# Optimization experiments

Measured on AMD Instinct MI355X. Metric: run time of the kernel, lower is better.

## Reference

```python
import jax, jax.numpy as jnp
import numpy as np

D_MODEL = 1024
NUM_HEADS = 16
OUT_SHAPE = (64,)            # ControlGate `shape`; d_head = prod(OUT_SHAPE)
BANK_SIZE = 16
TOP_K = 2
BATCH, SEQ = 8, 4096
D_OUT = NUM_HEADS * int(np.prod(OUT_SHAPE))  # 1024


def setup_inputs() -> dict:
    key = jax.random.key(0)
    k1, k2, k3, k4 = jax.random.split(key, 4)
    tensor = jax.random.normal(k1, (BATCH, SEQ, D_MODEL), dtype=jnp.float32)
    sel_idx = jax.random.randint(k2, (BATCH, TOP_K), 0, BANK_SIZE)
    sel_probs = jax.random.uniform(k3, (BATCH, TOP_K), dtype=jnp.float32)
    sel_probs = sel_probs / jnp.sum(sel_probs, axis=-1, keepdims=True)
    W = jax.random.normal(k4, (BANK_SIZE, D_MODEL, D_OUT), dtype=jnp.float32) * 0.02
    b = jnp.zeros((BANK_SIZE, D_OUT), dtype=jnp.float32)
    return {"tensor": tensor, "sel_idx": sel_idx, "sel_probs": sel_probs, "W": W, "b": b}


def reference(tensor, sel_idx, sel_probs, W, b):
    # --- VirtualMakeHeads: bank-selected (virtual) linear projection ---
    # Superimpose the selected weight banks per batch element.
    W_sel = W[sel_idx]                    # (B, K, d_model, d_out)  irregular gather
    b_sel = b[sel_idx]                    # (B, K, d_out)
    W_eff = jnp.einsum('bk,bkio->bio', sel_probs, W_sel)   # (B, d_model, d_out)
    b_eff = jnp.einsum('bk,bko->bo', sel_probs, b_sel)     # (B, d_out)
    logits = jnp.einsum('bsi,bio->bso', tensor, W_eff) + b_eff[:, None, :]
    # reshape to heads: (B, S, num_heads, d_head)
    logits = logits.reshape(*logits.shape[:-1], NUM_HEADS, -1)
    # --- ControlGate: unflatten last dim into OUT_SHAPE ---
    logits = logits.reshape(*logits.shape[:-1], *OUT_SHAPE)
    # DropoutLogits with p=0.0 (eval) is identity.
    # activation == 'sigmoid'
    return jax.nn.sigmoid(logits)
```

## Files before the change

kernel.cpp:

```cpp
#include <hip/hip_runtime.h>
#include <hip/hip_bf16.h>

#define B_  8
#define S_  4096
#define DM  1024
#define DO  1024

typedef __attribute__((ext_vector_type(4))) float f32x4;
typedef __attribute__((ext_vector_type(8))) short bf16x8;

__device__ inline unsigned int pkbf(float a, float b) {
    __hip_bfloat162 h = __float22bfloat162_rn(float2{a, b});
    union { __hip_bfloat162 h2; unsigned int u; } cv;
    cv.h2 = h;
    return cv.u;
}


__global__ __launch_bounds__(256) void prep_xpack(
    const float* __restrict__ X, unsigned short* __restrict__ xpack)
{
    const int kt = blockIdx.x, bm = blockIdx.y, b = blockIdx.z;
    const int r = threadIdx.x;
    const float* src = X + ((size_t)(b * S_ + bm * 256 + r)) * DM + kt * 64;
    char* dst = (char*)xpack + ((size_t)((b * 16 + bm) * 16 + kt)) * 32768 + r * 128;
    const int rx = r & 7;
    #pragma unroll
    for (int g = 0; g < 8; ++g) {
        float4 a = *reinterpret_cast<const float4*>(src + g * 8);
        float4 c = *reinterpret_cast<const float4*>(src + g * 8 + 4);
        uint4 u;
        u.x = pkbf(a.x, a.y); u.y = pkbf(a.z, a.w);
        u.z = pkbf(c.x, c.y); u.w = pkbf(c.z, c.w);
        *reinterpret_cast<uint4*>(dst + ((g ^ rx) << 4)) = u;
    }
}

__global__ __launch_bounds__(256) void prep_wpack64(
    const float* __restrict__ W, const int* __restrict__ sel_idx,
    const float* __restrict__ sel_probs, unsigned short* __restrict__ wpack)
{
    const int kt = blockIdx.x, nb = blockIdx.y, b = blockIdx.z;
    const int i0 = sel_idx[b*2+0], i1 = sel_idx[b*2+1];
    const float p0 = sel_probs[b*2+0], p1 = sel_probs[b*2+1];
    const int c = threadIdx.x;
    const int o = nb * 256 + c;
    const float* w0 = W + (size_t)i0 * DM * DO + (size_t)(kt * 64) * DO + o;
    const float* w1 = W + (size_t)i1 * DM * DO + (size_t)(kt * 64) * DO + o;
    char* dst = (char*)wpack + ((size_t)((b * 4 + nb) * 16 + kt)) * 32768 + c * 128;
    const int cx = c & 7;
    #pragma unroll
    for (int g = 0; g < 8; ++g) {
        float v[8];
        #pragma unroll
        for (int j = 0; j < 8; ++j)
            v[j] = p0 * w0[(size_t)(g * 8 + j) * DO] + p1 * w1[(size_t)(g * 8 + j) * DO];
        uint4 u;
        u.x = pkbf(v[0], v[1]); u.y = pkbf(v[2], v[3]);
        u.z = pkbf(v[4], v[5]); u.w = pkbf(v[6], v[7]);
        *reinterpret_cast<uint4*>(dst + ((g ^ cx) << 4)) = u;
    }
}

__global__ __launch_bounds__(256) void prep_beff(
    const float* __restrict__ bias, const int* __restrict__ sel_idx,
    const float* __restrict__ sel_probs, float* __restrict__ beff)
{
    const int b = blockIdx.x;
    const int i0 = sel_idx[b*2+0], i1 = sel_idx[b*2+1];
    const float p0 = sel_probs[b*2+0], p1 = sel_probs[b*2+1];
    for (int o = threadIdx.x; o < DO; o += blockDim.x)
        beff[(size_t)b * DO + o] = p0 * bias[(size_t)i0 * DO + o]
                                 + p1 * bias[(size_t)i1 * DO + o];
}

__global__ __launch_bounds__(512, 1) void gemmx(
    const unsigned short* __restrict__ xpack, const unsigned short* __restrict__ wpack,
    const float* __restrict__ beff, float* __restrict__ out)
{
    extern __shared__ char lds[];

    const int id = blockIdx.x;
    const int swz = (id & 7) * 64 + (id >> 3);
    const int b  = swz >> 6;
    const int bm = (swz >> 2) & 15;
    const int nb = swz & 3;

    const int t = threadIdx.x;
    const int wave = t >> 6, lane = t & 63;
    const int wm = wave >> 2, wnw = wave & 3;
    const int fr = lane & 15, fq = lane >> 4;

    const char* xt = (const char*)xpack + ((size_t)((b * 16 + bm) * 16)) * 32768;
    const char* wt = (const char*)wpack + ((size_t)((b * 4 + nb) * 16)) * 32768;

    const int s0 = ((fq ^ (fr & 7)) << 4);
    const int s1 = (((4 + fq) ^ (fr & 7)) << 4);
    const int rdA = wm * 16384 + fr * 128;
    const int rdB = wnw * 8192 + fr * 128;

    f32x4 acc[8][4] = {};
    bf16x8 afA[4], afB[4], afC[4], afD[4], bkA[4], bkB[4];

#define GLOAD(SRC, DSTOFF, I)                                                 \
    __builtin_amdgcn_global_load_lds(                                         \
        (const __attribute__((address_space(1))) void*)((SRC) + wave*4096 + (I)*1024 + lane*16), \
        (__attribute__((address_space(3))) void*)(lds + (DSTOFF) + wave*4096 + (I)*1024), 16, 0, 0)

#define MFMA16(MB, AF, BK)                                                    \
    __builtin_amdgcn_s_setprio(1);                                            \
    _Pragma("unroll")                                                         \
    for (int m = 0; m < 4; ++m) {                                             \
        _Pragma("unroll")                                                     \
        for (int nf = 0; nf < 4; ++nf)                                        \
            acc[(MB)+m][nf] = __builtin_amdgcn_mfma_f32_16x16x32_bf16(        \
                AF[m], BK[nf], acc[(MB)+m][nf], 0, 0, 0);                     \
    }                                                                         \
    __builtin_amdgcn_s_setprio(0);

#define READ_A(DST, BUF, MB, SK)                                              \
    _Pragma("unroll")                                                         \
    for (int m = 0; m < 4; ++m)                                               \
        DST[m] = *reinterpret_cast<const bf16x8*>(lds + (BUF) + rdA + ((MB)+m)*2048 + (SK));

#define READ_B(DST, BUF, SK)                                                  \
    _Pragma("unroll")                                                         \
    for (int nf = 0; nf < 4; ++nf)                                            \
        DST[nf] = *reinterpret_cast<const bf16x8*>(lds + (BUF) + rdB + nf*2048 + (SK));

    #pragma unroll
    for (int i = 0; i < 4; ++i) { GLOAD(xt, 0, i); GLOAD(wt, 65536, i); }
    asm volatile("s_waitcnt vmcnt(0)" ::: "memory");
    __builtin_amdgcn_s_barrier();
    READ_A(afA, 0, 0, s0);
    READ_B(bkA, 65536, s0);

    #pragma unroll 1
    for (int kt = 0; kt < 16; ++kt) {
        const int ca  = (kt & 1) * 32768;
        const int cb  = 65536 + ca;
        const int na  = 32768 - ca;
        const int nbf = 65536 + na;

        if (kt < 15) {
            const char* gxn = xt + (size_t)(kt + 1) * 32768;
            const char* gwn = wt + (size_t)(kt + 1) * 32768;
            #pragma unroll
            for (int i = 0; i < 4; ++i) { GLOAD(gxn, na, i); GLOAD(gwn, nbf, i); }
        }

        READ_A(afB, ca, 4, s0);
        MFMA16(0, afA, bkA)

        READ_B(bkB, cb, s1);
        READ_A(afC, ca, 0, s1);
        MFMA16(4, afB, bkA)

        READ_A(afD, ca, 4, s1);
        MFMA16(0, afC, bkB)

        asm volatile("s_waitcnt lgkmcnt(0)" ::: "memory");
        if (kt < 15) { asm volatile("s_waitcnt vmcnt(0)" ::: "memory"); }
        __builtin_amdgcn_s_barrier();

        if (kt < 15) {
            READ_A(afA, na, 0, s0);
            READ_B(bkA, nbf, s0);
        }
        MFMA16(4, afD, bkB)
    }

    const float* be = beff + (size_t)b * DO + nb * 256 + wnw * 64;
    float bv[4];
    #pragma unroll
    for (int nf = 0; nf < 4; ++nf) bv[nf] = be[nf * 16 + fr];

    float* ob = out + ((size_t)(b * S_ + bm * 256 + wm * 128)) * DO + nb * 256 + wnw * 64;
    #pragma unroll
    for (int mf = 0; mf < 8; ++mf) {
        #pragma unroll
        for (int nf = 0; nf < 4; ++nf) {
            const int col = nf * 16 + fr;
            #pragma unroll
            for (int r = 0; r < 4; ++r) {
                const int row = mf * 16 + fq * 4 + r;
                const float xv = acc[mf][nf][r] + bv[nf];
                ob[(size_t)row * DO + col] = 1.0f / (1.0f + __expf(-xv));
            }
        }
    }
#undef GLOAD
#undef MFMA16
#undef READ_A
#undef READ_B
}

__global__ __launch_bounds__(256) void prep_wpack_f(
    const float* __restrict__ W, const int* __restrict__ sel_idx,
    const float* __restrict__ sel_probs, unsigned short* __restrict__ wpack)
{
    const int kt = blockIdx.x, nb = blockIdx.y, b = blockIdx.z;
    const int i0 = sel_idx[b*2+0], i1 = sel_idx[b*2+1];
    const float p0 = sel_probs[b*2+0], p1 = sel_probs[b*2+1];
    const int t = threadIdx.x;
    const int col = t & 127;
    const int gh  = t >> 7;
    const int o = nb * 128 + col;
    const float* w0 = W + (size_t)i0 * DM * DO + (size_t)(kt * 32) * DO + o;
    const float* w1 = W + (size_t)i1 * DM * DO + (size_t)(kt * 32) * DO + o;
    char* tile = (char*)wpack + ((size_t)((b * 8 + nb) * 32 + kt)) * 8192;
    const int q = (col >> 1) & 3;
    #pragma unroll
    for (int gg = 0; gg < 2; ++gg) {
        const int g = gh * 2 + gg;
        float v[8];
        #pragma unroll
        for (int j = 0; j < 8; ++j)
            v[j] = p0 * w0[(size_t)(g * 8 + j) * DO] + p1 * w1[(size_t)(g * 8 + j) * DO];
        uint4 u;
        u.x = pkbf(v[0], v[1]); u.y = pkbf(v[2], v[3]);
        u.z = pkbf(v[4], v[5]); u.w = pkbf(v[6], v[7]);
        *reinterpret_cast<uint4*>(tile + col * 64 + ((g ^ q) << 4)) = u;
    }
}

__global__ __launch_bounds__(256, 4) void gemm4(
    const float* __restrict__ X, const unsigned short* __restrict__ wpack,
    const float* __restrict__ beff, float* __restrict__ out)
{
    __shared__ char lds[32768];
    const int id = blockIdx.x;
    const int swz = (id & 7) * 256 + (id >> 3);
    const int b  = swz >> 8;
    const int bm = (swz >> 3) & 31;
    const int nb = swz & 7;
    const int t = threadIdx.x;
    const int wave = t >> 6, lane = t & 63;
    const int wm = wave >> 1, wn = wave & 1;
    const int fr = lane & 15, fq = lane >> 4;
    const int s_row = t >> 1;
    const int s_h   = t & 1;
    const float* xrow = X + ((size_t)(b * S_ + bm * 128 + s_row)) * DM + s_h * 16;
    const int sq = (s_row >> 1) & 3;
    const int wrA0 = s_row * 64 + (((s_h * 2 + 0) ^ sq) << 4);
    const int wrA1 = s_row * 64 + (((s_h * 2 + 1) ^ sq) << 4);
    const char* wtile = (const char*)wpack + ((size_t)((b * 8 + nb) * 32)) * 8192;
    const int axor = (fr >> 1) & 3;
    const int rdA = (wm * 64 + fr) * 64 + ((fq ^ axor) << 4);
    const int rdB = (wn * 64 + fr) * 64 + ((fq ^ axor) << 4);
    f32x4 acc[4][4] = {};
    float4 ax0, ax1, ax2, ax3;
#define LOAD_X(KT)                                                            \
    {   const float* s = xrow + (KT) * 32;                                    \
        ax0 = *reinterpret_cast<const float4*>(s);                            \
        ax1 = *reinterpret_cast<const float4*>(s + 4);                        \
        ax2 = *reinterpret_cast<const float4*>(s + 8);                        \
        ax3 = *reinterpret_cast<const float4*>(s + 12); }
#define STAGE_B(KT, BOFF)                                                     \
    {   const char* gB = wtile + (size_t)(KT) * 8192;                         \
        _Pragma("unroll")                                                     \
        for (int r = 0; r < 2; ++r)                                           \
            __builtin_amdgcn_global_load_lds(                                 \
                (const __attribute__((address_space(1))) void*)(gB + (wave*2+r)*1024 + lane*16), \
                (__attribute__((address_space(3))) void*)(lds + (BOFF) + (wave*2+r)*1024),       \
                16, 0, 0); }
#define WRITE_A(AOFF)                                                         \
    {   uint4 u0, u1;                                                         \
        u0.x = pkbf(ax0.x, ax0.y); u0.y = pkbf(ax0.z, ax0.w);                 \
        u0.z = pkbf(ax1.x, ax1.y); u0.w = pkbf(ax1.z, ax1.w);                 \
        u1.x = pkbf(ax2.x, ax2.y); u1.y = pkbf(ax2.z, ax2.w);                 \
        u1.z = pkbf(ax3.x, ax3.y); u1.w = pkbf(ax3.z, ax3.w);                 \
        *reinterpret_cast<uint4*>(lds + (AOFF) + wrA0) = u0;                  \
        *reinterpret_cast<uint4*>(lds + (AOFF) + wrA1) = u1; }
    LOAD_X(0);
    __builtin_amdgcn_sched_barrier(0);
    STAGE_B(0, 16384);
    __builtin_amdgcn_sched_barrier(0);
    WRITE_A(0);
    __syncthreads();
    for (int kt = 0; kt < 32; ++kt) {
        const int cur = (kt & 1) * 8192;
        const int nxt = 8192 - cur;
        if (kt < 31) {
            LOAD_X(kt + 1);
            __builtin_amdgcn_sched_barrier(0);
            STAGE_B(kt + 1, 16384 + nxt);
            __builtin_amdgcn_sched_barrier(0);
        }
        bf16x8 bf[4];
        #pragma unroll
        for (int nf = 0; nf < 4; ++nf)
            bf[nf] = *reinterpret_cast<const bf16x8*>(lds + 16384 + cur + rdB + nf * 1024);
        #pragma unroll
        for (int m = 0; m < 4; ++m) {
            bf16x8 af = *reinterpret_cast<const bf16x8*>(lds + cur + rdA + m * 1024);
            #pragma unroll
            for (int nf = 0; nf < 4; ++nf)
                acc[m][nf] = __builtin_amdgcn_mfma_f32_16x16x32_bf16(af, bf[nf], acc[m][nf], 0, 0, 0);
        }
        if (kt < 31) { WRITE_A(nxt); }
        __syncthreads();
    }
    const float* be = beff + (size_t)b * DO + nb * 128 + wn * 64;
    float bv[4];
    #pragma unroll
    for (int nf = 0; nf < 4; ++nf) bv[nf] = be[nf * 16 + fr];
    float* ob = out + ((size_t)(b * S_ + bm * 128 + wm * 64)) * DO + nb * 128 + wn * 64;
    #pragma unroll
    for (int m = 0; m < 4; ++m) {
        #pragma unroll
        for (int nf = 0; nf < 4; ++nf) {
            const int col = nf * 16 + fr;
            #pragma unroll
            for (int r = 0; r < 4; ++r) {
                const int row = m * 16 + fq * 4 + r;
                const float xv = acc[m][nf][r] + bv[nf];
                ob[(size_t)row * DO + col] = 1.0f / (1.0f + __expf(-xv));
            }
        }
    }
#undef LOAD_X
#undef STAGE_B
#undef WRITE_A
}

extern "C" void kernel_launch(void* const* d_in, const int* in_sizes, int n_in,
                              void* d_out, int out_size, void* d_ws, size_t ws_size,
                              hipStream_t stream) {
    const float* tensor    = (const float*)d_in[0];
    const int*   sel_idx   = (const int*)d_in[1];
    const float* sel_probs = (const float*)d_in[2];
    const float* W         = (const float*)d_in[3];
    const float* bias      = (const float*)d_in[4];
    float* out = (float*)d_out;

    const size_t XP = (size_t)2048 * 32768;
    const size_t WP = (size_t)512 * 32768;
    const size_t NEED = XP + WP + (size_t)B_ * DO * 4;

    if (ws_size >= NEED) {
        unsigned short* xpack = (unsigned short*)d_ws;
        unsigned short* wpack = (unsigned short*)((char*)d_ws + XP);
        float* beff = (float*)((char*)d_ws + XP + WP);

        hipFuncSetAttribute((const void*)gemmx,
                            hipFuncAttributeMaxDynamicSharedMemorySize, 131072);

        hipLaunchKernelGGL(prep_xpack, dim3(16, 16, 8), dim3(256), 0, stream,
                           tensor, xpack);
        hipLaunchKernelGGL(prep_wpack64, dim3(16, 4, 8), dim3(256), 0, stream,
                           W, sel_idx, sel_probs, wpack);
        hipLaunchKernelGGL(prep_beff, dim3(8), dim3(256), 0, stream,
                           bias, sel_idx, sel_probs, beff);
        hipLaunchKernelGGL(gemmx, dim3(512), dim3(512), 131072, stream,
                           xpack, wpack, beff, out);
    } else {
        unsigned short* wpack = (unsigned short*)d_ws;
        float* beff = (float*)((char*)d_ws + (size_t)8 * 8 * 32 * 8192);
        hipLaunchKernelGGL(prep_wpack_f, dim3(32, 8, 8), dim3(256), 0, stream,
                           W, sel_idx, sel_probs, wpack);
        hipLaunchKernelGGL(prep_beff, dim3(8), dim3(256), 0, stream,
                           bias, sel_idx, sel_probs, beff);
        hipLaunchKernelGGL(gemm4, dim3(2048), dim3(256), 0, stream,
                           tensor, wpack, beff, out);
    }
}
```

Measured before the change: 150.7 us.

## Restructure bf16 GEMM into four-stage K=32 LDS ring pipeline

```diff
diff --git a/kernel.cpp b/kernel.cpp
--- a/kernel.cpp
+++ b/kernel.cpp
@@ -22,21 +22,21 @@
 {
     const int kt = blockIdx.x, bm = blockIdx.y, b = blockIdx.z;
     const int r = threadIdx.x;
-    const float* src = X + ((size_t)(b * S_ + bm * 256 + r)) * DM + kt * 64;
-    char* dst = (char*)xpack + ((size_t)((b * 16 + bm) * 16 + kt)) * 32768 + r * 128;
-    const int rx = r & 7;
-    #pragma unroll
-    for (int g = 0; g < 8; ++g) {
+    const float* src = X + ((size_t)(b * S_ + bm * 256 + r)) * DM + kt * 32;
+    char* dst = (char*)xpack + ((size_t)((b * 16 + bm) * 32 + kt)) * 16384 + r * 64;
+    const int q = (r >> 1) & 3;
+    #pragma unroll
+    for (int g = 0; g < 4; ++g) {
         float4 a = *reinterpret_cast<const float4*>(src + g * 8);
         float4 c = *reinterpret_cast<const float4*>(src + g * 8 + 4);
         uint4 u;
         u.x = pkbf(a.x, a.y); u.y = pkbf(a.z, a.w);
         u.z = pkbf(c.x, c.y); u.w = pkbf(c.z, c.w);
-        *reinterpret_cast<uint4*>(dst + ((g ^ rx) << 4)) = u;
-    }
-}
-
-__global__ __launch_bounds__(256) void prep_wpack64(
+        *reinterpret_cast<uint4*>(dst + ((g ^ q) << 4)) = u;
+    }
+}
+
+__global__ __launch_bounds__(256) void prep_wpack32(
     const float* __restrict__ W, const int* __restrict__ sel_idx,
     const float* __restrict__ sel_probs, unsigned short* __restrict__ wpack)
 {
@@ -45,12 +45,12 @@
     const float p0 = sel_probs[b*2+0], p1 = sel_probs[b*2+1];
     const int c = threadIdx.x;
     const int o = nb * 256 + c;
-    const float* w0 = W + (size_t)i0 * DM * DO + (size_t)(kt * 64) * DO + o;
-    const float* w1 = W + (size_t)i1 * DM * DO + (size_t)(kt * 64) * DO + o;
-    char* dst = (char*)wpack + ((size_t)((b * 4 + nb) * 16 + kt)) * 32768 + c * 128;
-    const int cx = c & 7;
-    #pragma unroll
-    for (int g = 0; g < 8; ++g) {
+    const float* w0 = W + (size_t)i0 * DM * DO + (size_t)(kt * 32) * DO + o;
+    const float* w1 = W + (size_t)i1 * DM * DO + (size_t)(kt * 32) * DO + o;
+    char* dst = (char*)wpack + ((size_t)((b * 4 + nb) * 32 + kt)) * 16384 + c * 64;
+    const int q = (c >> 1) & 3;
+    #pragma unroll
+    for (int g = 0; g < 4; ++g) {
         float v[8];
         #pragma unroll
         for (int j = 0; j < 8; ++j)
@@ -58,7 +58,7 @@
         uint4 u;
         u.x = pkbf(v[0], v[1]); u.y = pkbf(v[2], v[3]);
         u.z = pkbf(v[4], v[5]); u.w = pkbf(v[6], v[7]);
-        *reinterpret_cast<uint4*>(dst + ((g ^ cx) << 4)) = u;
+        *reinterpret_cast<uint4*>(dst + ((g ^ q) << 4)) = u;
     }
 }
 
@@ -74,7 +74,7 @@
                                  + p1 * bias[(size_t)i1 * DO + o];
 }
 
-__global__ __launch_bounds__(512, 1) void gemmx(
+__global__ __launch_bounds__(512, 2) void gemmr(
     const unsigned short* __restrict__ xpack, const unsigned short* __restrict__ wpack,
     const float* __restrict__ beff, float* __restrict__ out)
 {
@@ -91,84 +91,88 @@
     const int wm = wave >> 2, wnw = wave & 3;
     const int fr = lane & 15, fq = lane >> 4;
 
-    const char* xt = (const char*)xpack + ((size_t)((b * 16 + bm) * 16)) * 32768;
-    const char* wt = (const char*)wpack + ((size_t)((b * 4 + nb) * 16)) * 32768;
-
-    const int s0 = ((fq ^ (fr & 7)) << 4);
-    const int s1 = (((4 + fq) ^ (fr & 7)) << 4);
-    const int rdA = wm * 16384 + fr * 128;
-    const int rdB = wnw * 8192 + fr * 128;
+    const char* xt = (const char*)xpack + ((size_t)((b * 16 + bm) * 32)) * 16384;
+    const char* wt = (const char*)wpack + ((size_t)((b * 4 + nb) * 32)) * 16384;
+
+    const int q   = (fr >> 1) & 3;
+    const int rdA = (wm * 128 + fr) * 64 + ((fq ^ q) << 4);
+    const int rdB = (wnw * 64 + fr) * 64 + ((fq ^ q) << 4);
 
     f32x4 acc[8][4] = {};
-    bf16x8 afA[4], afB[4], afC[4], afD[4], bkA[4], bkB[4];
-
-#define GLOAD(SRC, DSTOFF, I)                                                 \
-    __builtin_amdgcn_global_load_lds(                                         \
-        (const __attribute__((address_space(1))) void*)((SRC) + wave*4096 + (I)*1024 + lane*16), \
-        (__attribute__((address_space(3))) void*)(lds + (DSTOFF) + wave*4096 + (I)*1024), 16, 0, 0)
-
-#define MFMA16(MB, AF, BK)                                                    \
-    __builtin_amdgcn_s_setprio(1);                                            \
-    _Pragma("unroll")                                                         \
-    for (int m = 0; m < 4; ++m) {                                             \
-        _Pragma("unroll")                                                     \
-        for (int nf = 0; nf < 4; ++nf)                                        \
-            acc[(MB)+m][nf] = __builtin_amdgcn_mfma_f32_16x16x32_bf16(        \
-                AF[m], BK[nf], acc[(MB)+m][nf], 0, 0, 0);                     \
-    }                                                                         \
+    bf16x8 afLo[4], afHi[4], bkA[4], bkB[4];
+
+#define GLOAD(SRC, DST)                                                        \
+    __builtin_amdgcn_global_load_lds(                                          \
+        (const __attribute__((address_space(1))) void*)(SRC),                  \
+        (__attribute__((address_space(3))) void*)(DST), 16, 0, 0)
+
+#define STAGE(KT, SLOT)                                                        \
+    {   const char* ga = xt + (size_t)(KT) * 16384 + wave * 2048 + lane * 16;  \
+        const char* gb = wt + (size_t)(KT) * 16384 + wave * 2048 + lane * 16;  \
+        char* la = lds + (SLOT) + wave * 2048;                                 \
+        char* lb = lds + 65536 + (SLOT) + wave * 2048;                         \
+        GLOAD(ga, la); GLOAD(ga + 1024, la + 1024);                            \
+        GLOAD(gb, lb); GLOAD(gb + 1024, lb + 1024); }
+
+#define READ_BK(DST, SLOT)                                                     \
+    _Pragma("unroll")                                                          \
+    for (int nf = 0; nf < 4; ++nf)                                             \
+        DST[nf] = *reinterpret_cast<const bf16x8*>(lds + 65536 + (SLOT) + rdB + nf * 1024);
+
+#define READ_ALO(SLOT)                                                         \
+    _Pragma("unroll")                                                          \
+    for (int m = 0; m < 4; ++m)                                                \
+        afLo[m] = *reinterpret_cast<const bf16x8*>(lds + (SLOT) + rdA + m * 1024);
+
+#define READ_AHI(SLOT)                                                         \
+    _Pragma("unroll")                                                          \
+    for (int m = 0; m < 4; ++m)                                                \
+        afHi[m] = *reinterpret_cast<const bf16x8*>(lds + (SLOT) + rdA + (4 + m) * 1024);
+
+#define MFMA16(MB, AF, BK)                                                     \
+    __builtin_amdgcn_s_setprio(1);                                             \
+    _Pragma("unroll")                                                          \
+    for (int m = 0; m < 4; ++m) {                                              \
+        _Pragma("unroll")                                                      \
+        for (int nf = 0; nf < 4; ++nf)                                         \
+            acc[(MB)+m][nf] = __builtin_amdgcn_mfma_f32_16x16x32_bf16(         \
+                AF[m], BK[nf], acc[(MB)+m][nf], 0, 0, 0);                      \
+    }                                                                          \
     __builtin_amdgcn_s_setprio(0);
 
-#define READ_A(DST, BUF, MB, SK)                                              \
-    _Pragma("unroll")                                                         \
-    for (int m = 0; m < 4; ++m)                                               \
-        DST[m] = *reinterpret_cast<const bf16x8*>(lds + (BUF) + rdA + ((MB)+m)*2048 + (SK));
-
-#define READ_B(DST, BUF, SK)                                                  \
-    _Pragma("unroll")                                                         \
-    for (int nf = 0; nf < 4; ++nf)                                            \
-        DST[nf] = *reinterpret_cast<const bf16x8*>(lds + (BUF) + rdB + nf*2048 + (SK));
-
-    #pragma unroll
-    for (int i = 0; i < 4; ++i) { GLOAD(xt, 0, i); GLOAD(wt, 65536, i); }
-    asm volatile("s_waitcnt vmcnt(0)" ::: "memory");
+#define SB0 __builtin_amdgcn_sched_barrier(0)
+
+#define BODY(KT, BKC, BKN, WAITN, DO_STAGE)                                    \
+    {   if (DO_STAGE) { STAGE((KT) + 3, (((KT) + 3) & 3) * 16384); }           \
+        SB0;                                                                   \
+        MFMA16(0, afLo, BKC)                                                   \
+        SB0;                                                                   \
+        asm volatile("s_waitcnt vmcnt(" #WAITN ") lgkmcnt(0)" ::: "memory");   \
+        __builtin_amdgcn_s_barrier();                                          \
+        {   const int sN = (((KT) + 1) & 3) * 16384;                           \
+            READ_BK(BKN, sN);                                                  \
+            READ_ALO(sN);                                                      \
+            SB0;                                                               \
+            MFMA16(4, afHi, BKC)                                               \
+            READ_AHI(sN); } }
+
+    STAGE(0, 0); STAGE(1, 16384); STAGE(2, 32768);
+    asm volatile("s_waitcnt vmcnt(8)" ::: "memory");
     __builtin_amdgcn_s_barrier();
-    READ_A(afA, 0, 0, s0);
-    READ_B(bkA, 65536, s0);
+    READ_BK(bkA, 0);
+    READ_ALO(0);
+    READ_AHI(0);
 
     #pragma unroll 1
-    for (int kt = 0; kt < 16; ++kt) {
-        const int ca  = (kt & 1) * 32768;
-        const int cb  = 65536 + ca;
-        const int na  = 32768 - ca;
-        const int nbf = 65536 + na;
-
-        if (kt < 15) {
-            const char* gxn = xt + (size_t)(kt + 1) * 32768;
-            const char* gwn = wt + (size_t)(kt + 1) * 32768;
-            #pragma unroll
-            for (int i = 0; i < 4; ++i) { GLOAD(gxn, na, i); GLOAD(gwn, nbf, i); }
-        }
-
-        READ_A(afB, ca, 4, s0);
-        MFMA16(0, afA, bkA)
-
-        READ_B(bkB, cb, s1);
-        READ_A(afC, ca, 0, s1);
-        MFMA16(4, afB, bkA)
-
-        READ_A(afD, ca, 4, s1);
-        MFMA16(0, afC, bkB)
-
-        asm volatile("s_waitcnt lgkmcnt(0)" ::: "memory");
-        if (kt < 15) { asm volatile("s_waitcnt vmcnt(0)" ::: "memory"); }
-        __builtin_amdgcn_s_barrier();
-
-        if (kt < 15) {
-            READ_A(afA, na, 0, s0);
-            READ_B(bkA, nbf, s0);
-        }
-        MFMA16(4, afD, bkB)
-    }
+    for (int kt = 0; kt < 28; kt += 2) {
+        BODY(kt,     bkA, bkB, 8, true)
+        BODY(kt + 1, bkB, bkA, 8, true)
+    }
+    BODY(28, bkA, bkB, 8, true)
+    BODY(29, bkB, bkA, 4, false)
+    BODY(30, bkA, bkB, 0, false)
+    MFMA16(0, afLo, bkB)
+    MFMA16(4, afHi, bkB)
 
     const float* be = beff + (size_t)b * DO + nb * 256 + wnw * 64;
     float bv[4];
@@ -190,9 +194,13 @@
         }
     }
 #undef GLOAD
+#undef STAGE
+#undef READ_BK
+#undef READ_ALO
+#undef READ_AHI
 #undef MFMA16
-#undef READ_A
-#undef READ_B
+#undef SB0
+#undef BODY
 }
 
 __global__ __launch_bounds__(256) void prep_wpack_f(
@@ -334,8 +342,8 @@
     const float* bias      = (const float*)d_in[4];
     float* out = (float*)d_out;
 
-    const size_t XP = (size_t)2048 * 32768;
-    const size_t WP = (size_t)512 * 32768;
+    const size_t XP = (size_t)4096 * 16384;
+    const size_t WP = (size_t)1024 * 16384;
     const size_t NEED = XP + WP + (size_t)B_ * DO * 4;
 
     if (ws_size >= NEED) {
@@ -343,16 +351,16 @@
         unsigned short* wpack = (unsigned short*)((char*)d_ws + XP);
         float* beff = (float*)((char*)d_ws + XP + WP);
 
-        hipFuncSetAttribute((const void*)gemmx,
+        hipFuncSetAttribute((const void*)gemmr,
                             hipFuncAttributeMaxDynamicSharedMemorySize, 131072);
 
-        hipLaunchKernelGGL(prep_xpack, dim3(16, 16, 8), dim3(256), 0, stream,
+        hipLaunchKernelGGL(prep_xpack, dim3(32, 16, 8), dim3(256), 0, stream,
                            tensor, xpack);
-        hipLaunchKernelGGL(prep_wpack64, dim3(16, 4, 8), dim3(256), 0, stream,
+        hipLaunchKernelGGL(prep_wpack32, dim3(32, 4, 8), dim3(256), 0, stream,
                            W, sel_idx, sel_probs, wpack);
         hipLaunchKernelGGL(prep_beff, dim3(8), dim3(256), 0, stream,
                            bias, sel_idx, sel_probs, beff);
-        hipLaunchKernelGGL(gemmx, dim3(512), dim3(512), 131072, stream,
+        hipLaunchKernelGGL(gemmr, dim3(512), dim3(512), 131072, stream,
                            xpack, wpack, beff, out);
     } else {
         unsigned short* wpack = (unsigned short*)d_ws;
```

After: 152.1 us. Within noise of the previous version (+0.9%).
